# Kernel tuning notes

Measured on AMD Instinct MI355X. Metric: run time of the kernel, lower is better.

The kernel has to match this reference:

```python
import jax, jax.numpy as jnp
import numpy as np

T, B, N = 16, 32, 4096
NUM_TYPES = 20
F = NUM_TYPES + 5  # 4 geo feats + one-hot type + valid flag
H = 8              # poly_hidden_layers
HID = 128          # hidden_layers


def _w(k, i, o):
    return jax.random.normal(k, (i, o), jnp.float32) / np.sqrt(i)


def setup_inputs() -> dict:
    key = jax.random.key(0)
    ks = jax.random.split(key, 8)
    points = jax.random.normal(ks[0], (T, B, N, F), jnp.float32)
    return {
        "points": points,
        "W1": _w(ks[1], F, H), "b1": jnp.zeros((H,), jnp.float32),
        "W2": _w(ks[2], H, H), "b2": jnp.zeros((H,), jnp.float32),
        "W3": _w(ks[3], H, H), "b3": jnp.zeros((H,), jnp.float32),
        "W4": _w(ks[4], 2 * H, H), "b4": jnp.zeros((H,), jnp.float32),
        "W5": _w(ks[5], H, H), "b5": jnp.zeros((H,), jnp.float32),
        "W6": _w(ks[6], H, H), "b6": jnp.zeros((H,), jnp.float32),
        "Wout": _w(ks[7], NUM_TYPES * H, HID), "bout": jnp.zeros((HID,), jnp.float32),
    }


def reference(points, W1, b1, W2, b2, W3, b3, W4, b4, W5, b5, W6, b6, Wout, bout):
    t, b, n, f = points.shape
    nt = f - 5
    x = points.reshape(t * b * n, f)
    valid = (x[:, -1:] != 0)                      # (TBN,1) nonzero == True, as jnp.where on floats
    types = jnp.argmax(x[:, 4:-1], axis=1)        # (TBN,) polyline type per point

    h = jax.nn.relu(x @ W1 + b1)
    h = jax.nn.relu(h @ W2 + b2)
    h = jax.nn.relu(h @ W3 + b3)
    h = jnp.where(valid, h, 0.0)                  # zero-out invalid points

    # segment id = (t,b) slot * num_types + type; pooling is per (t,b,type)
    tb = jnp.arange(t * b * n) // n
    seg = tb * nt + types
    num_seg = t * b * nt
    # original masks non-matching points to 0 then takes max over N; since h >= 0
    # (relu + zero masking), that equals max(segment_max, 0); empty types -> 0.
    pooled = jnp.maximum(jax.ops.segment_max(h, seg, num_segments=num_seg), 0.0)

    h = jnp.concatenate([h, pooled[seg]], axis=-1)  # (TBN, 2H)
    h = jax.nn.relu(h @ W4 + b4)
    h = jax.nn.relu(h @ W5 + b5)
    h = jax.nn.relu(h @ W6 + b6)
    h = jnp.where(valid, h, 0.0)

    pooled2 = jnp.maximum(jax.ops.segment_max(h, seg, num_segments=num_seg), 0.0)
    out = pooled2.reshape(t, b, nt * h.shape[-1])   # types concatenated along feature dim
    return jax.nn.relu(out @ Wout + bout)           # (T, B, hidden_layers)
```

## Files before the change

kernel.cpp:

```cpp
#include <hip/hip_runtime.h>

#define T_ 16
#define B_ 32
#define N_ 4096
#define NT 20
#define F_ 25
#define H_ 8
#define HID_ 128
#define PSTR 9
#define SEGF_ (NT*H_)
#define BT 512
#define NSUB (N_/BT)
#define CF (BT*F_)
#define WSL 1600

typedef __attribute__((address_space(1))) const void GV;
typedef __attribute__((address_space(3))) void LV;

__device__ __forceinline__ void g2l16(const float* g, float* l) {
  __builtin_amdgcn_global_load_lds((GV*)g, (LV*)l, 16, 0, 0);
}
__device__ __forceinline__ void g2l4(const float* g, float* l) {
  __builtin_amdgcn_global_load_lds((GV*)g, (LV*)l, 4, 0, 0);
}

__device__ __forceinline__ unsigned f2bf(float x) {
  unsigned u = __float_as_uint(x);
  u += 0x7fffu + ((u >> 16) & 1u);
  return u >> 16;
}
__device__ __forceinline__ float bf2f(unsigned s) { return __uint_as_float(s << 16); }

template<int NI>
__device__ __forceinline__ void layer(const float* in, const float* __restrict__ W,
                                      const float* __restrict__ b, float* out) {
#pragma unroll
  for (int j = 0; j < H_; j++) {
    float a = b[j];
#pragma unroll
    for (int f = 0; f < NI; f++) a = fmaf(in[f], W[f*H_ + j], a);
    out[j] = fmaxf(a, 0.0f);
  }
}

extern "C" __global__ __launch_bounds__(BT, 4)
void kFused(const float* __restrict__ pts,
            const float* __restrict__ W1, const float* __restrict__ b1,
            const float* __restrict__ W2, const float* __restrict__ b2,
            const float* __restrict__ W3, const float* __restrict__ b3,
            const float* __restrict__ W4, const float* __restrict__ b4,
            const float* __restrict__ W5, const float* __restrict__ b5,
            const float* __restrict__ W6, const float* __restrict__ b6,
            const float* __restrict__ Wout, const float* __restrict__ bout,
            float* __restrict__ out)
{
  __shared__ float xs[CF];
  __shared__ int lp1[NT*PSTR];
  __shared__ int lp2[NT*PSTR];
  const int tid  = threadIdx.x;
  const int wid  = tid >> 6;
  const int lane = tid & 63;
  const int tb = blockIdx.x;
  if (tid < NT*PSTR) { lp1[tid] = 0; lp2[tid] = 0; }
  __syncthreads();

  const float* base = pts + (size_t)tb * (N_*F_);
  float* lw = xs + wid*WSL;

#define ISSUE(S)                                                         \
  {                                                                      \
    const float* gw = base + (S)*CF + wid*WSL;                           \
    _Pragma("unroll")                                                    \
    for (int k = 0; k < 6; k++)                                          \
      g2l16(gw + k*256 + lane*4, lw + k*256 + lane*4);                   \
    g2l4(gw + 1536 + lane, lw + 1536 + lane);                            \
  }

  uint4 h3p[NSUB];
  int   tyv[NSUB];

  ISSUE(0)

#define PH1(S)                                                           \
  {                                                                      \
    asm volatile("s_waitcnt vmcnt(0)" ::: "memory");                     \
    __builtin_amdgcn_sched_barrier(0);                                   \
    float xv[F_];                                                        \
    _Pragma("unroll")                                                    \
    for (int f = 0; f < F_; f++) xv[f] = lw[lane*F_ + f];                \
    asm volatile("s_waitcnt lgkmcnt(0)" ::: "memory");                   \
    __builtin_amdgcn_sched_barrier(0);                                   \
    if ((S) < NSUB-1) ISSUE((S)+1)                                       \
    int ty = 0; float best = xv[4];                                      \
    _Pragma("unroll")                                                    \
    for (int k = 1; k < NT; k++)                                         \
      if (xv[4+k] > best) { best = xv[4+k]; ty = k; }                    \
    const bool valid = (xv[F_-1] != 0.0f);                               \
    float t1[H_], t2[H_];                                                \
    layer<F_>(xv, W1, b1, t1);                                           \
    layer<H_>(t1, W2, b2, t2);                                           \
    layer<H_>(t2, W3, b3, t1);                                           \
    if (!valid) {                                                        \
      _Pragma("unroll")                                                  \
      for (int j = 0; j < H_; j++) t1[j] = 0.0f;                         \
    }                                                                    \
    h3p[S].x = f2bf(t1[0]) | (f2bf(t1[1]) << 16);                        \
    h3p[S].y = f2bf(t1[2]) | (f2bf(t1[3]) << 16);                        \
    h3p[S].z = f2bf(t1[4]) | (f2bf(t1[5]) << 16);                        \
    h3p[S].w = f2bf(t1[6]) | (f2bf(t1[7]) << 16);                        \
    tyv[S] = valid ? ty : -1;                                            \
    if (valid) {                                                         \
      _Pragma("unroll")                                                  \
      for (int j = 0; j < H_; j++)                                       \
        atomicMax(&lp1[ty*PSTR + j], __float_as_int(t1[j]));             \
    }                                                                    \
  }

  PH1(0) PH1(1) PH1(2) PH1(3) PH1(4) PH1(5) PH1(6) PH1(7)

  __syncthreads();

#define PH2(S)                                                           \
  {                                                                      \
    const int ty = tyv[S];                                               \
    if (ty >= 0) {                                                       \
      float x16[2*H_];                                                   \
      x16[0] = bf2f(h3p[S].x & 0xffffu); x16[1] = bf2f(h3p[S].x >> 16);  \
      x16[2] = bf2f(h3p[S].y & 0xffffu); x16[3] = bf2f(h3p[S].y >> 16);  \
      x16[4] = bf2f(h3p[S].z & 0xffffu); x16[5] = bf2f(h3p[S].z >> 16);  \
      x16[6] = bf2f(h3p[S].w & 0xffffu); x16[7] = bf2f(h3p[S].w >> 16);  \
      _Pragma("unroll")                                                  \
      for (int j = 0; j < H_; j++)                                       \
        x16[H_+j] = __int_as_float(lp1[ty*PSTR + j]);                    \
      float t1[H_], t2[H_];                                              \
      layer<2*H_>(x16, W4, b4, t1);                                      \
      layer<H_>(t1, W5, b5, t2);                                         \
      layer<H_>(t2, W6, b6, t1);                                         \
      _Pragma("unroll")                                                  \
      for (int j = 0; j < H_; j++)                                       \
        atomicMax(&lp2[ty*PSTR + j], __float_as_int(t1[j]));             \
    }                                                                    \
  }

  PH2(0) PH2(1) PH2(2) PH2(3) PH2(4) PH2(5) PH2(6) PH2(7)

  __syncthreads();

  if (tid < HID_) {
    float a = bout[tid];
#pragma unroll 4
    for (int k = 0; k < SEGF_; k++) {
      const float v = __int_as_float(lp2[(k >> 3)*PSTR + (k & 7)]);
      a = fmaf(v, Wout[k*HID_ + tid], a);
    }
    out[tb*HID_ + tid] = fmaxf(a, 0.0f);
  }
#undef ISSUE
#undef PH1
#undef PH2
}

extern "C" void kernel_launch(void* const* d_in, const int* in_sizes, int n_in,
                              void* d_out, int out_size, void* d_ws, size_t ws_size,
                              hipStream_t stream) {
  const float* pts  = (const float*)d_in[0];
  const float* W1   = (const float*)d_in[1];  const float* b1 = (const float*)d_in[2];
  const float* W2   = (const float*)d_in[3];  const float* b2 = (const float*)d_in[4];
  const float* W3   = (const float*)d_in[5];  const float* b3 = (const float*)d_in[6];
  const float* W4   = (const float*)d_in[7];  const float* b4 = (const float*)d_in[8];
  const float* W5   = (const float*)d_in[9];  const float* b5 = (const float*)d_in[10];
  const float* W6   = (const float*)d_in[11]; const float* b6 = (const float*)d_in[12];
  const float* Wout = (const float*)d_in[13]; const float* bout = (const float*)d_in[14];
  float* out = (float*)d_out;

  kFused<<<T_*B_, BT, 0, stream>>>(pts, W1, b1, W2, b2, W3, b3,
                                   W4, b4, W5, b5, W6, b6, Wout, bout, out);
}
```

Measured before the change: 65.87 us.

## Use packed FMA, hardware bf16 pack, and precompute per-type pooled contribution

New measurement: 62.51 us, median of 2. 5.1% less time.

```diff
diff --git a/kernel.cpp b/kernel.cpp
--- a/kernel.cpp
+++ b/kernel.cpp
@@ -24,22 +24,53 @@
   __builtin_amdgcn_global_load_lds((GV*)g, (LV*)l, 4, 0, 0);
 }
 
-__device__ __forceinline__ unsigned f2bf(float x) {
-  unsigned u = __float_as_uint(x);
-  u += 0x7fffu + ((u >> 16) & 1u);
-  return u >> 16;
-}
 __device__ __forceinline__ float bf2f(unsigned s) { return __uint_as_float(s << 16); }
 
+__device__ __forceinline__ unsigned cvtpk_bf16(float lo, float hi) {
+  unsigned r;
+  asm("v_cvt_pk_bf16_f32 %0, %1, %2" : "=v"(r) : "v"(lo), "v"(hi));
+  return r;
+}
+
+__device__ __forceinline__ void pkfma(float2& acc, float a,
+                                      const float* __restrict__ wp) {
+  const float2 w = *(const float2*)wp;
+  float2 a2; a2.x = a; a2.y = a;
+  asm("v_pk_fma_f32 %0, %1, %2, %0" : "+v"(acc) : "v"(a2), "s"(w));
+}
+
 template<int NI>
-__device__ __forceinline__ void layer(const float* in, const float* __restrict__ W,
-                                      const float* __restrict__ b, float* out) {
-#pragma unroll
-  for (int j = 0; j < H_; j++) {
-    float a = b[j];
-#pragma unroll
-    for (int f = 0; f < NI; f++) a = fmaf(in[f], W[f*H_ + j], a);
-    out[j] = fmaxf(a, 0.0f);
+__device__ __forceinline__ void layerP(const float* in, const float* __restrict__ W,
+                                       const float* __restrict__ b, float* out) {
+  float2 acc[4];
+#pragma unroll
+  for (int jp = 0; jp < 4; jp++) acc[jp] = *(const float2*)&b[jp*2];
+#pragma unroll
+  for (int f = 0; f < NI; f++) {
+#pragma unroll
+    for (int jp = 0; jp < 4; jp++) pkfma(acc[jp], in[f], &W[f*H_ + jp*2]);
+  }
+#pragma unroll
+  for (int jp = 0; jp < 4; jp++) {
+    out[jp*2]   = fmaxf(acc[jp].x, 0.0f);
+    out[jp*2+1] = fmaxf(acc[jp].y, 0.0f);
+  }
+}
+
+__device__ __forceinline__ void layerPc(const float* in, const float* __restrict__ W,
+                                        const float* ctbp, float* out) {
+  float2 acc[4];
+#pragma unroll
+  for (int jp = 0; jp < 4; jp++) acc[jp] = *(const float2*)&ctbp[jp*2];
+#pragma unroll
+  for (int f = 0; f < H_; f++) {
+#pragma unroll
+    for (int jp = 0; jp < 4; jp++) pkfma(acc[jp], in[f], &W[f*H_ + jp*2]);
+  }
+#pragma unroll
+  for (int jp = 0; jp < 4; jp++) {
+    out[jp*2]   = fmaxf(acc[jp].x, 0.0f);
+    out[jp*2+1] = fmaxf(acc[jp].y, 0.0f);
   }
 }
 
@@ -54,9 +85,10 @@
             const float* __restrict__ Wout, const float* __restrict__ bout,
             float* __restrict__ out)
 {
-  __shared__ float xs[CF];
+  __shared__ float xs[8*WSL];
   __shared__ int lp1[NT*PSTR];
   __shared__ int lp2[NT*PSTR];
+  __shared__ float ctb[NT*H_];
   const int tid  = threadIdx.x;
   const int wid  = tid >> 6;
   const int lane = tid & 63;
@@ -97,17 +129,17 @@
       if (xv[4+k] > best) { best = xv[4+k]; ty = k; }                    \
     const bool valid = (xv[F_-1] != 0.0f);                               \
     float t1[H_], t2[H_];                                                \
-    layer<F_>(xv, W1, b1, t1);                                           \
-    layer<H_>(t1, W2, b2, t2);                                           \
-    layer<H_>(t2, W3, b3, t1);                                           \
+    layerP<F_>(xv, W1, b1, t1);                                          \
+    layerP<H_>(t1, W2, b2, t2);                                          \
+    layerP<H_>(t2, W3, b3, t1);                                          \
     if (!valid) {                                                        \
       _Pragma("unroll")                                                  \
       for (int j = 0; j < H_; j++) t1[j] = 0.0f;                         \
     }                                                                    \
-    h3p[S].x = f2bf(t1[0]) | (f2bf(t1[1]) << 16);                        \
-    h3p[S].y = f2bf(t1[2]) | (f2bf(t1[3]) << 16);                        \
-    h3p[S].z = f2bf(t1[4]) | (f2bf(t1[5]) << 16);                        \
-    h3p[S].w = f2bf(t1[6]) | (f2bf(t1[7]) << 16);                        \
+    h3p[S].x = cvtpk_bf16(t1[0], t1[1]);                                 \
+    h3p[S].y = cvtpk_bf16(t1[2], t1[3]);                                 \
+    h3p[S].z = cvtpk_bf16(t1[4], t1[5]);                                 \
+    h3p[S].w = cvtpk_bf16(t1[6], t1[7]);                                 \
     tyv[S] = valid ? ty : -1;                                            \
     if (valid) {                                                         \
       _Pragma("unroll")                                                  \
@@ -120,22 +152,29 @@
 
   __syncthreads();
 
+  if (tid < NT*H_) {
+    const int cty = tid >> 3, cj = tid & 7;
+    float a = b4[cj];
+#pragma unroll
+    for (int k = 0; k < H_; k++)
+      a = fmaf(__int_as_float(lp1[cty*PSTR + k]), W4[(H_+k)*H_ + cj], a);
+    ctb[tid] = a;
+  }
+  __syncthreads();
+
 #define PH2(S)                                                           \
   {                                                                      \
     const int ty = tyv[S];                                               \
     if (ty >= 0) {                                                       \
-      float x16[2*H_];                                                   \
-      x16[0] = bf2f(h3p[S].x & 0xffffu); x16[1] = bf2f(h3p[S].x >> 16);  \
-      x16[2] = bf2f(h3p[S].y & 0xffffu); x16[3] = bf2f(h3p[S].y >> 16);  \
-      x16[4] = bf2f(h3p[S].z & 0xffffu); x16[5] = bf2f(h3p[S].z >> 16);  \
-      x16[6] = bf2f(h3p[S].w & 0xffffu); x16[7] = bf2f(h3p[S].w >> 16);  \
-      _Pragma("unroll")                                                  \
-      for (int j = 0; j < H_; j++)                                       \
-        x16[H_+j] = __int_as_float(lp1[ty*PSTR + j]);                    \
+      float x8[H_];                                                      \
+      x8[0] = bf2f(h3p[S].x & 0xffffu); x8[1] = bf2f(h3p[S].x >> 16);    \
+      x8[2] = bf2f(h3p[S].y & 0xffffu); x8[3] = bf2f(h3p[S].y >> 16);    \
+      x8[4] = bf2f(h3p[S].z & 0xffffu); x8[5] = bf2f(h3p[S].z >> 16);    \
+      x8[6] = bf2f(h3p[S].w & 0xffffu); x8[7] = bf2f(h3p[S].w >> 16);    \
       float t1[H_], t2[H_];                                              \
-      layer<2*H_>(x16, W4, b4, t1);                                      \
-      layer<H_>(t1, W5, b5, t2);                                         \
-      layer<H_>(t2, W6, b6, t1);                                         \
+      layerPc(x8, W4, &ctb[ty*H_], t1);                                  \
+      layerP<H_>(t1, W5, b5, t2);                                        \
+      layerP<H_>(t2, W6, b6, t1);                                        \
       _Pragma("unroll")                                                  \
       for (int j = 0; j < H_; j++)                                       \
         atomicMax(&lp2[ty*PSTR + j], __float_as_int(t1[j]));             \
```
